# Performance work log

Hardware: AMD Instinct MI355X
Metric: run time of the kernel (lower is better)

The kernel has to match this reference:

```python
import jax, jax.numpy as jnp
import numpy as np

EPS = 1e-5  # BatchNorm eps


def _bn(x, g, b, axes):
    # training-mode batch norm over `axes`, channel dim broadcast via g/b shape
    m = jnp.mean(x, axis=axes, keepdims=True)
    v = jnp.var(x, axis=axes, keepdims=True)
    shape = [1] * x.ndim
    ch_axis = [a for a in range(x.ndim) if a not in axes][0]
    shape[ch_axis] = g.shape[0]
    return g.reshape(shape) * (x - m) * jax.lax.rsqrt(v + EPS) + b.reshape(shape)


def setup_inputs() -> dict:
    key = jax.random.key(0)
    ks = jax.random.split(key, 8)
    B, C, N = 16, 3, 2048

    def w(k_, fan_in, fan_out):
        return jax.random.normal(k_, (fan_in, fan_out), jnp.float32) * (1.0 / np.sqrt(fan_in))

    return {
        "pc": jax.random.normal(ks[0], (B, C, N), jnp.float32),
        "W1": w(ks[1], 6, 64), "g1": jnp.ones(64), "b1": jnp.zeros(64),
        "W2": w(ks[2], 64, 128), "g2": jnp.ones(128), "b2": jnp.zeros(128),
        "W3": w(ks[3], 128, 1024), "g3": jnp.ones(1024), "b3": jnp.zeros(1024),
        "Wf1": w(ks[4], 1024, 512), "gf1": jnp.ones(512), "bf1": jnp.zeros(512),
        "Wf2": w(ks[5], 512, 256), "gf2": jnp.ones(256), "bf2": jnp.zeros(256),
        "Wf3": jnp.zeros((256, 9), jnp.float32),           # zero-initialized per source
        "bf3": jnp.eye(3, dtype=jnp.float32).reshape(-1),  # identity bias per source
        "k": 20,
    }


def reference(pc, W1, g1, b1, W2, g2, b2, W3, g3, b3,
              Wf1, gf1, bf1, Wf2, gf2, bf2, Wf3, bf3, k):
    B, C, N = pc.shape
    # ---- KNN graph on coordinates (B x C x N) ----
    sq = jnp.sum(pc * pc, axis=1)                      # B,N
    inner = jnp.einsum('bcn,bcm->bnm', pc, pc)         # B,N,N
    negdist = 2.0 * inner - sq[:, :, None] - sq[:, None, :]
    _, idx = jax.lax.top_k(negdist, k)                 # B,N,k (includes self)
    # gather neighbor features: f (C,N), i (N,k) -> (C,N,k)
    topk = jax.vmap(lambda f, i: f[:, i])(pc, idx)     # B,C,N,k
    center = pc[:, :, :, None]
    edge = jnp.concatenate(
        [jnp.broadcast_to(center, topk.shape), topk - center], axis=1)  # B,2C,N,k

    # ---- edge conv (1x1 conv + BN + ReLU), pool=False ----
    h = jnp.einsum('bcnk,co->bonk', edge, W1)
    h = jax.nn.relu(_bn(h, g1, b1, (0, 2, 3)))         # B,64,N,k
    # ---- conv2 then max over k ----
    h = jnp.einsum('bcnk,co->bonk', h, W2)
    h = jax.nn.relu(_bn(h, g2, b2, (0, 2, 3)))         # B,128,N,k
    h = jnp.max(h, axis=-1)                            # B,128,N
    # ---- conv3 then max over N ----
    h = jnp.einsum('bcn,co->bon', h, W3)
    h = jax.nn.relu(_bn(h, g3, b3, (0, 2)))            # B,1024,N
    h = jnp.max(h, axis=-1)                            # B,1024
    # ---- FC stack ----
    h = jax.nn.relu(_bn(h @ Wf1, gf1, bf1, (0,)))      # B,512
    h = jax.nn.relu(_bn(h @ Wf2, gf2, bf2, (0,)))      # B,256
    h = h @ Wf3 + bf3                                  # B,9
    return h.reshape(B, 3, 3)
```

## Files before the change

kernel.cpp:

```cpp
#include <hip/hip_runtime.h>
#include <math.h>

#define Nn 2048

#define OFF_IDX    ((size_t)0)
#define OFF_P2MAX  (((size_t)4)  << 20)
#define OFF_P2MIN  (((size_t)13) << 20)
#define OFF_PS2    (((size_t)22) << 20)
#define OFF_PQ2    (((size_t)23) << 20)
#define OFF_STATS  (((size_t)24) << 20)
#define OFF_MOM    (OFF_STATS + 0)
#define OFF_A1C1   (OFF_STATS + 4096)
#define OFF_A2C2   (OFF_STATS + 8192)
#define OFF_S3SUM  (OFF_STATS + 12288)
#define OFF_S3SQ   (OFF_STATS + 20480)
#define OFF_P3MAX  (OFF_STATS + 28672)
#define OFF_P3MIN  (OFF_STATS + 94208)
#define OFF_R3     (OFF_STATS + 159744)
#define OFF_R4     (OFF_STATS + 225280)
#define OFF_R5     (OFF_STATS + 258048)
#define OFF_DOTS1  (OFF_STATS + 274432)
#define OFF_DOTS2  (OFF_STATS + 307200)
#define OFF_W2BF   (OFF_STATS + 323584)
#define OFF_W3BF   (OFF_STATS + 339968)
#define WS_NEEDED  (OFF_STATS + 602112)

typedef __attribute__((ext_vector_type(8))) short bf16x8;
typedef __attribute__((ext_vector_type(4))) float f32x4;

__device__ __forceinline__ unsigned fkey(float f){
  unsigned u = __float_as_uint(f);
  return (u & 0x80000000u) ? ~u : (u | 0x80000000u);
}
__device__ __forceinline__ float fdec(unsigned k){
  unsigned u = (k & 0x80000000u) ? (k & 0x7FFFFFFFu) : ~k;
  return __uint_as_float(u);
}
__device__ __forceinline__ short f2bf(float x){
  unsigned u = __float_as_uint(x);
  u += 0x7fffu + ((u >> 16) & 1u);
  return (short)(u >> 16);
}
__device__ __forceinline__ float bf2f(short v){
  return __uint_as_float(((unsigned)(unsigned short)v) << 16);
}
__device__ __forceinline__ float med3(float a, float b, float c){
  float d;
  asm("v_med3_f32 %0, %1, %2, %3" : "=v"(d) : "v"(a), "v"(b), "v"(c));
  return d;
}
__device__ __forceinline__ float ndist(float tQx, float tQy, float tQz, float Qw, float4 P){
  return fmaf(tQx, P.x, fmaf(tQy, P.y, fmaf(tQz, P.z, -Qw - P.w)));
}
__device__ __forceinline__ void insert20(float (&m)[20], float x){
  #pragma unroll
  for (int t = 0; t < 19; t++) m[t] = med3(m[t], m[t+1], x);
  m[19] = fmaxf(m[19], x);
}

__global__ __launch_bounds__(256) void k_init(char* __restrict__ ws){
  int i = blockIdx.x*256 + threadIdx.x;
  if (i < 7168) ((unsigned*)(ws + OFF_MOM))[i] = 0u;
  if (i < 16384){
    ((unsigned*)(ws + OFF_P3MAX))[i] = 0u;
    ((unsigned*)(ws + OFF_P3MIN))[i] = 0xFFFFFFFFu;
  }
  if (i < 12288) ((float*)(ws + OFF_DOTS1))[i] = 0.f;
}

__global__ __launch_bounds__(256) void k_castw(const float* __restrict__ W2,
      const float* __restrict__ W3, short* __restrict__ W2BF,
      short* __restrict__ W3BF){
  int id = blockIdx.x*256 + threadIdx.x;
  if (id < 16384){
    int q = id >> 4, k0 = (id & 15)*8;
    bf16x8 vv;
    #pragma unroll
    for (int j = 0; j < 8; j++) vv[j] = f2bf(W3[(size_t)(k0+j)*1024 + q]);
    *(bf16x8*)&W3BF[q*128 + k0] = vv;
  } else if (id < 17408){
    int id2 = id - 16384;
    int q = id2 >> 3, k0 = (id2 & 7)*8;
    bf16x8 vv;
    #pragma unroll
    for (int j = 0; j < 8; j++) vv[j] = f2bf(W2[(k0+j)*128 + q]);
    *(bf16x8*)&W2BF[q*64 + k0] = vv;
  }
}

__global__ __launch_bounds__(512) void k_knn(const float* __restrict__ pc,
                                             int* __restrict__ idxg,
                                             double* __restrict__ MOM){
  __shared__ float4 pts[Nn];
  __shared__ unsigned cnt[64];
  __shared__ float momS[27];
  const int tid = threadIdx.x;
  const int b = blockIdx.y;
  const int n0 = blockIdx.x*64;
  const float* pcb = pc + b*3*Nn;
  for (int i = tid; i < Nn; i += 512){
    float x = pcb[i], y = pcb[Nn+i], z = pcb[2*Nn+i];
    pts[i] = make_float4(x, y, z, x*x + y*y + z*z);
  }
  if (tid < 64) cnt[tid] = 0u;
  if (tid < 27) momS[tid] = 0.f;
  __syncthreads();

  const int ql = tid >> 3, c = tid & 7;
  const int n = n0 + ql;
  const float4 Q = pts[n];
  const float tQx = 2.f*Q.x, tQy = 2.f*Q.y, tQz = 2.f*Q.z;

  float v[20];
  #pragma unroll
  for (int t = 0; t < 20; t++) v[t] = -3.4e38f;
  #pragma unroll 1
  for (int i = 0; i < 256; i += 4){
    float4 P0 = pts[(i+0)*8 + c];
    float4 P1 = pts[(i+1)*8 + c];
    float4 P2 = pts[(i+2)*8 + c];
    float4 P3 = pts[(i+3)*8 + c];
    insert20(v, ndist(tQx, tQy, tQz, Q.w, P0));
    insert20(v, ndist(tQx, tQy, tQz, Q.w, P1));
    insert20(v, ndist(tQx, tQy, tQz, Q.w, P2));
    insert20(v, ndist(tQx, tQy, tQz, Q.w, P3));
  }

  #pragma unroll
  for (int stage = 4; stage >= 1; stage >>= 1){
    float w[20];
    #pragma unroll
    for (int t = 0; t < 20; t++) w[t] = __shfl_xor(v[t], stage);
    #pragma unroll
    for (int t = 0; t < 20; t++) insert20(v, w[t]);
  }
  const float th = v[0];

  int* myidx = &idxg[((size_t)((b<<11) + n))*20];
  #pragma unroll 1
  for (int i = 0; i < 256; i += 4){
    float4 P0 = pts[(i+0)*8 + c];
    float4 P1 = pts[(i+1)*8 + c];
    float4 P2 = pts[(i+2)*8 + c];
    float4 P3 = pts[(i+3)*8 + c];
    float nd0 = ndist(tQx, tQy, tQz, Q.w, P0);
    float nd1 = ndist(tQx, tQy, tQz, Q.w, P1);
    float nd2 = ndist(tQx, tQy, tQz, Q.w, P2);
    float nd3 = ndist(tQx, tQy, tQz, Q.w, P3);
    if (nd0 >= th){ unsigned p = atomicAdd(&cnt[ql], 1u); if (p < 20u) myidx[p] = (i+0)*8 + c; }
    if (nd1 >= th){ unsigned p = atomicAdd(&cnt[ql], 1u); if (p < 20u) myidx[p] = (i+1)*8 + c; }
    if (nd2 >= th){ unsigned p = atomicAdd(&cnt[ql], 1u); if (p < 20u) myidx[p] = (i+2)*8 + c; }
    if (nd3 >= th){ unsigned p = atomicAdd(&cnt[ql], 1u); if (p < 20u) myidx[p] = (i+3)*8 + c; }
  }
  __threadfence_block();
  __syncthreads();

  if (c == 0){
    unsigned have = cnt[ql]; if (have > 20u) have = 20u;
    for (unsigned p = have; p < 20u; ++p) myidx[p] = n;
  }
  __threadfence_block();
  __syncthreads();

  float s1[6] = {0,0,0,0,0,0};
  float s2[21] = {0,0,0,0,0,0,0,0,0,0,0,0,0,0,0,0,0,0,0,0,0};
  #pragma unroll 1
  for (int j = tid; j < 1280; j += 512){
    int q = j/20, t = j - q*20;
    int m = idxg[((size_t)((b<<11) + n0 + q))*20 + t] & 2047;
    float4 P = pts[m];
    float4 Qq = pts[n0 + q];
    float e[6] = {Qq.x, Qq.y, Qq.z, P.x - Qq.x, P.y - Qq.y, P.z - Qq.z};
    int u = 0;
    #pragma unroll
    for (int a = 0; a < 6; a++){
      s1[a] += e[a];
      #pragma unroll
      for (int bq = a; bq < 6; bq++){ s2[u] += e[a]*e[bq]; u++; }
    }
  }
  #pragma unroll
  for (int a = 0; a < 6; a++)
    for (int off = 32; off > 0; off >>= 1) s1[a] += __shfl_xor(s1[a], off);
  #pragma unroll
  for (int u = 0; u < 21; u++)
    for (int off = 32; off > 0; off >>= 1) s2[u] += __shfl_xor(s2[u], off);
  if ((tid & 63) == 0){
    #pragma unroll
    for (int a = 0; a < 6; a++) atomicAdd(&momS[a], s1[a]);
    #pragma unroll
    for (int u = 0; u < 21; u++) atomicAdd(&momS[6+u], s2[u]);
  }
  __syncthreads();
  if (tid < 27) atomicAdd(&MOM[tid], (double)momS[tid]);
}

__global__ __launch_bounds__(64) void k_coef1(const double* __restrict__ MOM,
        const float* __restrict__ W1, const float* __restrict__ g1,
        const float* __restrict__ b1, float* __restrict__ A1C1){
  const int o = threadIdx.x;
  const double inv = 1.0/655360.0;
  double w[6]; double m = 0.0;
  #pragma unroll
  for (int c = 0; c < 6; c++){ w[c] = (double)W1[c*64+o]; m += w[c]*MOM[c]*inv; }
  double e2 = 0.0; int u = 0;
  #pragma unroll
  for (int c = 0; c < 6; c++){
    #pragma unroll
    for (int cp = c; cp < 6; cp++){
      double mm = MOM[6+u]*inv; u++;
      e2 += (c == cp) ? w[c]*w[c]*mm : 2.0*w[c]*w[cp]*mm;
    }
  }
  double var = e2 - m*m;
  double a = (double)g1[o] / sqrt(var + 1e-5);
  #pragma unroll
  for (int c = 0; c < 6; c++) A1C1[c*64+o] = (float)(a*w[c]);
  A1C1[384+o] = (float)((double)b1[o] - a*m);
}

__global__ __launch_bounds__(256) void k_conv12(const float* __restrict__ pc,
      const int* __restrict__ idxg, const float* __restrict__ A1C1,
      const short* __restrict__ W2BF,
      float* __restrict__ PS2, float* __restrict__ PQ2,
      short* __restrict__ P2MAX, short* __restrict__ P2MIN){
  __shared__ float es[6][512];
  __shared__ short h1s[512*64];
  __shared__ float w1s[448];
  __shared__ float ssum[128], ssq[128];
  const int tid = threadIdx.x;
  const int b = blockIdx.y;
  const int n0 = blockIdx.x*16;
  const float* pcb = pc + b*3*Nn;

  for (int i = tid; i < 448; i += 256) w1s[i] = A1C1[i];

  for (int s = tid; s < 512; s += 256){
    int nl = s >> 5, kk = s & 31;
    int n = n0 + nl;
    int kke = (kk < 20) ? kk : 0;
    int m = idxg[((size_t)((b<<11)+n))*20 + kke] & 2047;
    float cx = pcb[n],  cy = pcb[Nn+n],  cz = pcb[2*Nn+n];
    float px = pcb[m],  py = pcb[Nn+m],  pz = pcb[2*Nn+m];
    es[0][s] = cx;    es[1][s] = cy;    es[2][s] = cz;
    es[3][s] = px-cx; es[4][s] = py-cy; es[5][s] = pz-cz;
  }
  __syncthreads();

  for (int i = tid; i < 4096; i += 256){
    int s = i >> 3, oc = i & 7;
    bf16x8 hv;
    #pragma unroll
    for (int j = 0; j < 8; j++){
      int o = oc*8 + j;
      float acc = w1s[384 + o];
      #pragma unroll
      for (int c = 0; c < 6; c++) acc = fmaf(w1s[c*64 + o], es[c][s], acc);
      hv[j] = f2bf(fmaxf(acc, 0.f));
    }
    *(bf16x8*)&h1s[s*64 + ((oc ^ (s & 7)) << 3)] = hv;
  }
  __syncthreads();

  const int l = tid & 63, wv = tid >> 6;
  const int col = l & 15, kc = l >> 4;

  bf16x8 Bf[2][2];
  #pragma unroll
  for (int qt = 0; qt < 2; qt++){
    int q = wv*32 + qt*16 + col;
    #pragma unroll
    for (int ks = 0; ks < 2; ks++)
      Bf[qt][ks] = *(const bf16x8*)&W2BF[q*64 + ks*32 + kc*8];
  }

  float smacc[2] = {0.f, 0.f}, sqacc[2] = {0.f, 0.f};
  const bool t1real = (kc == 0);

  #pragma unroll 1
  for (int g = 0; g < 16; g++){
    bf16x8 Af[2][2];
    #pragma unroll
    for (int t = 0; t < 2; t++){
      int row = g*32 + t*16 + col;
      #pragma unroll
      for (int ks = 0; ks < 2; ks++){
        int chunk = (ks*4 + kc) ^ (row & 7);
        Af[t][ks] = *(const bf16x8*)&h1s[row*64 + chunk*8];
      }
    }
    #pragma unroll
    for (int qt = 0; qt < 2; qt++){
      f32x4 a0 = {0.f,0.f,0.f,0.f}, a1 = {0.f,0.f,0.f,0.f};
      a0 = __builtin_amdgcn_mfma_f32_16x16x32_bf16(Af[0][0], Bf[qt][0], a0, 0,0,0);
      a0 = __builtin_amdgcn_mfma_f32_16x16x32_bf16(Af[0][1], Bf[qt][1], a0, 0,0,0);
      a1 = __builtin_amdgcn_mfma_f32_16x16x32_bf16(Af[1][0], Bf[qt][0], a1, 0,0,0);
      a1 = __builtin_amdgcn_mfma_f32_16x16x32_bf16(Af[1][1], Bf[qt][1], a1, 0,0,0);
      float mx = a0[0], mn = a0[0], sm = 0.f, sq = 0.f;
      #pragma unroll
      for (int r = 0; r < 4; r++){
        float v0 = a0[r], v1 = a1[r];
        mx = fmaxf(mx, fmaxf(v0, v1));
        mn = fminf(mn, fminf(v0, v1));
        sm += v0; sq += v0*v0;
      }
      if (t1real){
        #pragma unroll
        for (int r = 0; r < 4; r++){ float v1 = a1[r]; sm += v1; sq += v1*v1; }
      }
      smacc[qt] += sm; sqacc[qt] += sq;
      mx = fmaxf(mx, __shfl_xor(mx, 16)); mx = fmaxf(mx, __shfl_xor(mx, 32));
      mn = fminf(mn, __shfl_xor(mn, 16)); mn = fminf(mn, __shfl_xor(mn, 32));
      if (kc == 0){
        size_t base = ((size_t)(b*Nn + n0 + g))*128 + (size_t)(wv*32 + qt*16 + col);
        P2MAX[base] = f2bf(mx);
        P2MIN[base] = f2bf(mn);
      }
    }
  }
  #pragma unroll
  for (int qt = 0; qt < 2; qt++){
    smacc[qt] += __shfl_xor(smacc[qt], 16); smacc[qt] += __shfl_xor(smacc[qt], 32);
    sqacc[qt] += __shfl_xor(sqacc[qt], 16); sqacc[qt] += __shfl_xor(sqacc[qt], 32);
    if (kc == 0){
      ssum[wv*32 + qt*16 + col] = smacc[qt];
      ssq [wv*32 + qt*16 + col] = sqacc[qt];
    }
  }
  __syncthreads();
  if (tid < 128){
    int bid = b*128 + blockIdx.x;
    PS2[tid*2048 + bid] = ssum[tid];
    PQ2[tid*2048 + bid] = ssq[tid];
  }
}

__global__ __launch_bounds__(256) void k_coef2(const float* __restrict__ PS2,
        const float* __restrict__ PQ2, const float* __restrict__ g2,
        const float* __restrict__ b2, float* __restrict__ A2C2){
  __shared__ float sred[4], qred[4];
  const int p = blockIdx.x;
  const int tid = threadIdx.x;
  float s = 0.f, q = 0.f;
  for (int i = tid; i < 2048; i += 256){ s += PS2[p*2048 + i]; q += PQ2[p*2048 + i]; }
  #pragma unroll
  for (int off = 32; off > 0; off >>= 1){ s += __shfl_xor(s, off); q += __shfl_xor(q, off); }
  if ((tid & 63) == 0){ sred[tid >> 6] = s; qred[tid >> 6] = q; }
  __syncthreads();
  if (tid == 0){
    double sum = (double)sred[0] + sred[1] + sred[2] + sred[3];
    double sq  = (double)qred[0] + qred[1] + qred[2] + qred[3];
    double mean = sum * (1.0/655360.0);
    double var  = sq  * (1.0/655360.0) - mean*mean;
    double a = (double)g2[p] / sqrt(var + 1e-5);
    A2C2[p]     = (float)a;
    A2C2[128+p] = (float)((double)b2[p] - a*mean);
  }
}

__global__ __launch_bounds__(256) void k_conv3(const short* __restrict__ P2MAX,
      const short* __restrict__ P2MIN, const float* __restrict__ A2C2,
      const short* __restrict__ W3BF, double* __restrict__ S3SUM,
      double* __restrict__ S3SQ, unsigned* __restrict__ P3MAX,
      unsigned* __restrict__ P3MIN){
  __shared__ short As[128*128];
  __shared__ float a2[128], c2[128];
  const int tid = threadIdx.x;
  const int b = blockIdx.y;
  const int n0 = blockIdx.x*128;
  const int qh = blockIdx.z;
  if (tid < 128){ a2[tid] = A2C2[tid]; c2[tid] = A2C2[128+tid]; }
  __syncthreads();

  for (int idx = tid; idx < 2048; idx += 256){
    int s = idx >> 4, oc = idx & 15;
    size_t base = ((size_t)(b*Nn + n0 + s))*128 + (size_t)(oc*8);
    bf16x8 vmx = *(const bf16x8*)&P2MAX[base];
    bf16x8 vmn = *(const bf16x8*)&P2MIN[base];
    bf16x8 vv;
    #pragma unroll
    for (int j = 0; j < 8; j++){
      int o = oc*8 + j;
      float aa = a2[o];
      float vsel = bf2f((aa >= 0.f) ? vmx[j] : vmn[j]);
      vv[j] = f2bf(fmaxf(aa*vsel + c2[o], 0.f));
    }
    int chunk = oc ^ (s & 7);
    *(bf16x8*)&As[s*128 + chunk*8] = vv;
  }
  __syncthreads();

  const int l = tid & 63, wv = tid >> 6;
  const int col = l & 15, kc = l >> 4;

  #pragma unroll 1
  for (int pass = 0; pass < 2; ++pass){
    bf16x8 Bf[4][4];
    #pragma unroll
    for (int qt = 0; qt < 4; qt++){
      int q = qh*512 + wv*128 + pass*64 + qt*16 + col;
      #pragma unroll
      for (int ks = 0; ks < 4; ks++)
        Bf[qt][ks] = *(const bf16x8*)&W3BF[q*128 + ks*32 + kc*8];
    }
    float smx[4], smn[4], ssm[4], ssqv[4];
    #pragma unroll
    for (int qt = 0; qt < 4; qt++){ smx[qt] = -3.4e38f; smn[qt] = 3.4e38f; ssm[qt] = 0.f; ssqv[qt] = 0.f; }

    #pragma unroll 1
    for (int st = 0; st < 8; ++st){
      bf16x8 Af[4];
      int row = st*16 + col;
      #pragma unroll
      for (int ks = 0; ks < 4; ks++){
        int chunk = (ks*4 + kc) ^ (row & 7);
        Af[ks] = *(const bf16x8*)&As[row*128 + chunk*8];
      }
      #pragma unroll
      for (int qt = 0; qt < 4; qt++){
        f32x4 acc = {0.f, 0.f, 0.f, 0.f};
        #pragma unroll
        for (int ks = 0; ks < 4; ks++)
          acc = __builtin_amdgcn_mfma_f32_16x16x32_bf16(Af[ks], Bf[qt][ks], acc, 0, 0, 0);
        #pragma unroll
        for (int r = 0; r < 4; r++){
          float vv = acc[r];
          smx[qt] = fmaxf(smx[qt], vv); smn[qt] = fminf(smn[qt], vv);
          ssm[qt] += vv; ssqv[qt] += vv*vv;
        }
      }
    }
    #pragma unroll
    for (int qt = 0; qt < 4; qt++){
      #pragma unroll
      for (int off = 16; off <= 32; off <<= 1){
        smx[qt] = fmaxf(smx[qt], __shfl_xor(smx[qt], off));
        smn[qt] = fminf(smn[qt], __shfl_xor(smn[qt], off));
        ssm[qt] += __shfl_xor(ssm[qt], off);
        ssqv[qt] += __shfl_xor(ssqv[qt], off);
      }
    }
    if (kc == 0){
      #pragma unroll
      for (int qt = 0; qt < 4; qt++){
        int q = qh*512 + wv*128 + pass*64 + qt*16 + col;
        atomicMax(&P3MAX[b*1024 + q], fkey(smx[qt]));
        atomicMin(&P3MIN[b*1024 + q], fkey(smn[qt]));
        atomicAdd(&S3SUM[q], (double)ssm[qt]);
        atomicAdd(&S3SQ[q],  (double)ssqv[qt]);
      }
    }
  }
}

__global__ __launch_bounds__(256) void k_bn3relu(const double* __restrict__ S3SUM,
      const double* __restrict__ S3SQ, const unsigned* __restrict__ P3MAX,
      const unsigned* __restrict__ P3MIN, const float* __restrict__ g3,
      const float* __restrict__ b3, float* __restrict__ R3){
  int id = blockIdx.x*256 + threadIdx.x;
  int q = id & 1023;
  double mean = S3SUM[q] * (1.0/32768.0);
  double var  = S3SQ[q] * (1.0/32768.0) - mean*mean;
  double a = (double)g3[q] / sqrt(var + 1e-5);
  double c = (double)b3[q] - a*mean;
  float v = fdec((a >= 0.0) ? P3MAX[id] : P3MIN[id]);
  R3[id] = fmaxf((float)(a*(double)v + c), 0.f);
}

template<int IN, int OUT>
__global__ __launch_bounds__(256) void k_fcdot(const float* __restrict__ X,
      const float* __restrict__ W, float* __restrict__ dots){
  constexpr int L = IN/16;
  __shared__ float Xs[16*L];
  const int tid = threadIdx.x;
  const int o = blockIdx.x*64 + (tid & 63);
  const int wv = tid >> 6;
  const int c0 = blockIdx.y*L;
  for (int i = tid; i < 16*L; i += 256){
    int bb = i / L, cc = i - bb*L;
    Xs[i] = X[bb*IN + c0 + cc];
  }
  __syncthreads();
  constexpr int CPW = L/4;
  float acc[16];
  #pragma unroll
  for (int bb = 0; bb < 16; bb++) acc[bb] = 0.f;
  for (int cc = wv*CPW; cc < (wv+1)*CPW; ++cc){
    float w = W[(size_t)(c0+cc)*OUT + o];
    #pragma unroll
    for (int bb = 0; bb < 16; bb++) acc[bb] += Xs[bb*L + cc]*w;
  }
  #pragma unroll
  for (int bb = 0; bb < 16; bb++) atomicAdd(&dots[bb*OUT + o], acc[bb]);
}

template<int OUT>
__global__ __launch_bounds__(64) void k_fcbn(const float* __restrict__ dots,
      const float* __restrict__ g, const float* __restrict__ bet,
      float* __restrict__ Y){
  const int o = blockIdx.x*64 + threadIdx.x;
  float d[16]; float m = 0.f;
  #pragma unroll
  for (int bb = 0; bb < 16; bb++){ d[bb] = dots[bb*OUT + o]; m += d[bb]; }
  m *= (1.f/16.f);
  float v = 0.f;
  #pragma unroll
  for (int bb = 0; bb < 16; bb++){ float x = d[bb]-m; v += x*x; }
  v *= (1.f/16.f);
  float a = g[o] * rsqrtf(v + 1e-5f);
  #pragma unroll
  for (int bb = 0; bb < 16; bb++) Y[bb*OUT + o] = fmaxf(a*(d[bb]-m) + bet[o], 0.f);
}

__global__ __launch_bounds__(192) void k_head(const float* __restrict__ R5,
      const float* __restrict__ Wf3, const float* __restrict__ bf3,
      float* __restrict__ out){
  int t = threadIdx.x;
  if (t >= 144) return;
  int b = t/9, j = t - b*9;
  float acc = bf3[j];
  for (int c = 0; c < 256; c++) acc += R5[b*256 + c]*Wf3[c*9 + j];
  out[t] = acc;
}

extern "C" void kernel_launch(void* const* d_in, const int* in_sizes, int n_in,
                              void* d_out, int out_size, void* d_ws, size_t ws_size,
                              hipStream_t stream) {
  if (ws_size < WS_NEEDED) return;
  const float* pc  = (const float*)d_in[0];
  const float* W1  = (const float*)d_in[1];
  const float* g1  = (const float*)d_in[2];
  const float* b1  = (const float*)d_in[3];
  const float* W2  = (const float*)d_in[4];
  const float* g2  = (const float*)d_in[5];
  const float* b2  = (const float*)d_in[6];
  const float* W3  = (const float*)d_in[7];
  const float* g3  = (const float*)d_in[8];
  const float* b3  = (const float*)d_in[9];
  const float* Wf1 = (const float*)d_in[10];
  const float* gf1 = (const float*)d_in[11];
  const float* bf1 = (const float*)d_in[12];
  const float* Wf2 = (const float*)d_in[13];
  const float* gf2 = (const float*)d_in[14];
  const float* bf2 = (const float*)d_in[15];
  const float* Wf3 = (const float*)d_in[16];
  const float* bf3 = (const float*)d_in[17];

  char* ws = (char*)d_ws;
  int*      IDX   = (int*)     (ws + OFF_IDX);
  short*    P2MAXp= (short*)   (ws + OFF_P2MAX);
  short*    P2MINp= (short*)   (ws + OFF_P2MIN);
  float*    PS2p  = (float*)   (ws + OFF_PS2);
  float*    PQ2p  = (float*)   (ws + OFF_PQ2);
  double*   MOMp  = (double*)  (ws + OFF_MOM);
  float*    A1C1p = (float*)   (ws + OFF_A1C1);
  float*    A2C2p = (float*)   (ws + OFF_A2C2);
  double*   S3SUMp= (double*)  (ws + OFF_S3SUM);
  double*   S3SQp = (double*)  (ws + OFF_S3SQ);
  unsigned* P3MAXp= (unsigned*)(ws + OFF_P3MAX);
  unsigned* P3MINp= (unsigned*)(ws + OFF_P3MIN);
  float*    R3p   = (float*)   (ws + OFF_R3);
  float*    R4p   = (float*)   (ws + OFF_R4);
  float*    R5p   = (float*)   (ws + OFF_R5);
  float*    DOTS1p= (float*)   (ws + OFF_DOTS1);
  float*    DOTS2p= (float*)   (ws + OFF_DOTS2);
  short*    W2BFp = (short*)   (ws + OFF_W2BF);
  short*    W3BFp = (short*)   (ws + OFF_W3BF);

  k_init          <<<dim3(64),       256, 0, stream>>>(ws);
  k_castw         <<<dim3(68),       256, 0, stream>>>(W2, W3, W2BFp, W3BFp);
  k_knn           <<<dim3(32,16),    512, 0, stream>>>(pc, IDX, MOMp);
  k_coef1         <<<dim3(1),         64, 0, stream>>>(MOMp, W1, g1, b1, A1C1p);
  k_conv12        <<<dim3(128,16),   256, 0, stream>>>(pc, IDX, A1C1p, W2BFp, PS2p, PQ2p, P2MAXp, P2MINp);
  k_coef2         <<<dim3(128),      256, 0, stream>>>(PS2p, PQ2p, g2, b2, A2C2p);
  k_conv3         <<<dim3(16,16,2),  256, 0, stream>>>(P2MAXp, P2MINp, A2C2p, W3BFp, S3SUMp, S3SQp, P3MAXp, P3MINp);
  k_bn3relu       <<<dim3(64),       256, 0, stream>>>(S3SUMp, S3SQp, P3MAXp, P3MINp, g3, b3, R3p);
  k_fcdot<1024,512><<<dim3(8,16),    256, 0, stream>>>(R3p, Wf1, DOTS1p);
  k_fcbn<512>     <<<dim3(8),         64, 0, stream>>>(DOTS1p, gf1, bf1, R4p);
  k_fcdot<512,256><<<dim3(4,16),     256, 0, stream>>>(R4p, Wf2, DOTS2p);
  k_fcbn<256>     <<<dim3(4),         64, 0, stream>>>(DOTS2p, gf2, bf2, R5p);
  k_head          <<<dim3(1),        192, 0, stream>>>(R5p, Wf3, bf3, (float*)d_out);
}
```

Baseline: 238.0 us.

## Fuse small kernels and halve conv12 shared-memory footprint via chunked h1

```diff
diff --git a/kernel.cpp b/kernel.cpp
--- a/kernel.cpp
+++ b/kernel.cpp
@@ -10,15 +10,11 @@
 #define OFF_PQ2    (((size_t)23) << 20)
 #define OFF_STATS  (((size_t)24) << 20)
 #define OFF_MOM    (OFF_STATS + 0)
-#define OFF_A1C1   (OFF_STATS + 4096)
 #define OFF_A2C2   (OFF_STATS + 8192)
 #define OFF_S3SUM  (OFF_STATS + 12288)
 #define OFF_S3SQ   (OFF_STATS + 20480)
 #define OFF_P3MAX  (OFF_STATS + 28672)
 #define OFF_P3MIN  (OFF_STATS + 94208)
-#define OFF_R3     (OFF_STATS + 159744)
-#define OFF_R4     (OFF_STATS + 225280)
-#define OFF_R5     (OFF_STATS + 258048)
 #define OFF_DOTS1  (OFF_STATS + 274432)
 #define OFF_DOTS2  (OFF_STATS + 307200)
 #define OFF_W2BF   (OFF_STATS + 323584)
@@ -58,7 +54,9 @@
   m[19] = fmaxf(m[19], x);
 }
 
-__global__ __launch_bounds__(256) void k_init(char* __restrict__ ws){
+__global__ __launch_bounds__(256) void k_setup(char* __restrict__ ws,
+      const float* __restrict__ W2, const float* __restrict__ W3,
+      short* __restrict__ W2BF, short* __restrict__ W3BF){
   int i = blockIdx.x*256 + threadIdx.x;
   if (i < 7168) ((unsigned*)(ws + OFF_MOM))[i] = 0u;
   if (i < 16384){
@@ -66,20 +64,14 @@
     ((unsigned*)(ws + OFF_P3MIN))[i] = 0xFFFFFFFFu;
   }
   if (i < 12288) ((float*)(ws + OFF_DOTS1))[i] = 0.f;
-}
-
-__global__ __launch_bounds__(256) void k_castw(const float* __restrict__ W2,
-      const float* __restrict__ W3, short* __restrict__ W2BF,
-      short* __restrict__ W3BF){
-  int id = blockIdx.x*256 + threadIdx.x;
-  if (id < 16384){
-    int q = id >> 4, k0 = (id & 15)*8;
+  if (i < 16384){
+    int q = i >> 4, k0 = (i & 15)*8;
     bf16x8 vv;
     #pragma unroll
     for (int j = 0; j < 8; j++) vv[j] = f2bf(W3[(size_t)(k0+j)*1024 + q]);
     *(bf16x8*)&W3BF[q*128 + k0] = vv;
-  } else if (id < 17408){
-    int id2 = id - 16384;
+  } else if (i < 17408){
+    int id2 = i - 16384;
     int q = id2 >> 3, k0 = (id2 & 7)*8;
     bf16x8 vv;
     #pragma unroll
@@ -195,37 +187,14 @@
   if (tid < 27) atomicAdd(&MOM[tid], (double)momS[tid]);
 }
 
-__global__ __launch_bounds__(64) void k_coef1(const double* __restrict__ MOM,
-        const float* __restrict__ W1, const float* __restrict__ g1,
-        const float* __restrict__ b1, float* __restrict__ A1C1){
-  const int o = threadIdx.x;
-  const double inv = 1.0/655360.0;
-  double w[6]; double m = 0.0;
-  #pragma unroll
-  for (int c = 0; c < 6; c++){ w[c] = (double)W1[c*64+o]; m += w[c]*MOM[c]*inv; }
-  double e2 = 0.0; int u = 0;
-  #pragma unroll
-  for (int c = 0; c < 6; c++){
-    #pragma unroll
-    for (int cp = c; cp < 6; cp++){
-      double mm = MOM[6+u]*inv; u++;
-      e2 += (c == cp) ? w[c]*w[c]*mm : 2.0*w[c]*w[cp]*mm;
-    }
-  }
-  double var = e2 - m*m;
-  double a = (double)g1[o] / sqrt(var + 1e-5);
-  #pragma unroll
-  for (int c = 0; c < 6; c++) A1C1[c*64+o] = (float)(a*w[c]);
-  A1C1[384+o] = (float)((double)b1[o] - a*m);
-}
-
 __global__ __launch_bounds__(256) void k_conv12(const float* __restrict__ pc,
-      const int* __restrict__ idxg, const float* __restrict__ A1C1,
-      const short* __restrict__ W2BF,
+      const int* __restrict__ idxg, const double* __restrict__ MOM,
+      const float* __restrict__ W1, const float* __restrict__ g1,
+      const float* __restrict__ b1, const short* __restrict__ W2BF,
       float* __restrict__ PS2, float* __restrict__ PQ2,
       short* __restrict__ P2MAX, short* __restrict__ P2MIN){
   __shared__ float es[6][512];
-  __shared__ short h1s[512*64];
+  __shared__ short h1s[256*64];
   __shared__ float w1s[448];
   __shared__ float ssum[128], ssq[128];
   const int tid = threadIdx.x;
@@ -233,7 +202,27 @@
   const int n0 = blockIdx.x*16;
   const float* pcb = pc + b*3*Nn;
 
-  for (int i = tid; i < 448; i += 256) w1s[i] = A1C1[i];
+  if (tid < 64){
+    const int o = tid;
+    const double inv = 1.0/655360.0;
+    double w[6]; double m = 0.0;
+    #pragma unroll
+    for (int cc = 0; cc < 6; cc++){ w[cc] = (double)W1[cc*64+o]; m += w[cc]*MOM[cc]*inv; }
+    double e2 = 0.0; int u = 0;
+    #pragma unroll
+    for (int cc = 0; cc < 6; cc++){
+      #pragma unroll
+      for (int cp = cc; cp < 6; cp++){
+        double mm = MOM[6+u]*inv; u++;
+        e2 += (cc == cp) ? w[cc]*w[cc]*mm : 2.0*w[cc]*w[cp]*mm;
+      }
+    }
+    double var = e2 - m*m;
+    double a = (double)g1[o] / sqrt(var + 1e-5);
+    #pragma unroll
+    for (int cc = 0; cc < 6; cc++) w1s[cc*64+o] = (float)(a*w[cc]);
+    w1s[384+o] = (float)((double)b1[o] - a*m);
+  }
 
   for (int s = tid; s < 512; s += 256){
     int nl = s >> 5, kk = s & 31;
@@ -247,21 +236,6 @@
   }
   __syncthreads();
 
-  for (int i = tid; i < 4096; i += 256){
-    int s = i >> 3, oc = i & 7;
-    bf16x8 hv;
-    #pragma unroll
-    for (int j = 0; j < 8; j++){
-      int o = oc*8 + j;
-      float acc = w1s[384 + o];
-      #pragma unroll
-      for (int c = 0; c < 6; c++) acc = fmaf(w1s[c*64 + o], es[c][s], acc);
-      hv[j] = f2bf(fmaxf(acc, 0.f));
-    }
-    *(bf16x8*)&h1s[s*64 + ((oc ^ (s & 7)) << 3)] = hv;
-  }
-  __syncthreads();
-
   const int l = tid & 63, wv = tid >> 6;
   const int col = l & 15, kc = l >> 4;
 
@@ -278,46 +252,68 @@
   const bool t1real = (kc == 0);
 
   #pragma unroll 1
-  for (int g = 0; g < 16; g++){
-    bf16x8 Af[2][2];
-    #pragma unroll
-    for (int t = 0; t < 2; t++){
-      int row = g*32 + t*16 + col;
-      #pragma unroll
-      for (int ks = 0; ks < 2; ks++){
-        int chunk = (ks*4 + kc) ^ (row & 7);
-        Af[t][ks] = *(const bf16x8*)&h1s[row*64 + chunk*8];
-      }
-    }
-    #pragma unroll
-    for (int qt = 0; qt < 2; qt++){
-      f32x4 a0 = {0.f,0.f,0.f,0.f}, a1 = {0.f,0.f,0.f,0.f};
-      a0 = __builtin_amdgcn_mfma_f32_16x16x32_bf16(Af[0][0], Bf[qt][0], a0, 0,0,0);
-      a0 = __builtin_amdgcn_mfma_f32_16x16x32_bf16(Af[0][1], Bf[qt][1], a0, 0,0,0);
-      a1 = __builtin_amdgcn_mfma_f32_16x16x32_bf16(Af[1][0], Bf[qt][0], a1, 0,0,0);
-      a1 = __builtin_amdgcn_mfma_f32_16x16x32_bf16(Af[1][1], Bf[qt][1], a1, 0,0,0);
-      float mx = a0[0], mn = a0[0], sm = 0.f, sq = 0.f;
-      #pragma unroll
-      for (int r = 0; r < 4; r++){
-        float v0 = a0[r], v1 = a1[r];
-        mx = fmaxf(mx, fmaxf(v0, v1));
-        mn = fminf(mn, fminf(v0, v1));
-        sm += v0; sq += v0*v0;
-      }
-      if (t1real){
+  for (int ch = 0; ch < 2; ch++){
+    for (int i = tid; i < 2048; i += 256){
+      int sl = i >> 3, oc = i & 7;
+      int s = (ch << 8) + sl;
+      bf16x8 hv;
+      #pragma unroll
+      for (int j = 0; j < 8; j++){
+        int o = oc*8 + j;
+        float acc = w1s[384 + o];
         #pragma unroll
-        for (int r = 0; r < 4; r++){ float v1 = a1[r]; sm += v1; sq += v1*v1; }
-      }
-      smacc[qt] += sm; sqacc[qt] += sq;
-      mx = fmaxf(mx, __shfl_xor(mx, 16)); mx = fmaxf(mx, __shfl_xor(mx, 32));
-      mn = fminf(mn, __shfl_xor(mn, 16)); mn = fminf(mn, __shfl_xor(mn, 32));
-      if (kc == 0){
-        size_t base = ((size_t)(b*Nn + n0 + g))*128 + (size_t)(wv*32 + qt*16 + col);
-        P2MAX[base] = f2bf(mx);
-        P2MIN[base] = f2bf(mn);
-      }
-    }
-  }
+        for (int cc = 0; cc < 6; cc++) acc = fmaf(w1s[cc*64 + o], es[cc][s], acc);
+        hv[j] = f2bf(fmaxf(acc, 0.f));
+      }
+      *(bf16x8*)&h1s[sl*64 + ((oc ^ (sl & 7)) << 3)] = hv;
+    }
+    __syncthreads();
+
+    #pragma unroll 1
+    for (int g2 = 0; g2 < 8; g2++){
+      const int g = ch*8 + g2;
+      bf16x8 Af[2][2];
+      #pragma unroll
+      for (int t = 0; t < 2; t++){
+        int rl = g2*32 + t*16 + col;
+        #pragma unroll
+        for (int ks = 0; ks < 2; ks++){
+          int chunk = (ks*4 + kc) ^ (rl & 7);
+          Af[t][ks] = *(const bf16x8*)&h1s[rl*64 + chunk*8];
+        }
+      }
+      #pragma unroll
+      for (int qt = 0; qt < 2; qt++){
+        f32x4 a0 = {0.f,0.f,0.f,0.f}, a1 = {0.f,0.f,0.f,0.f};
+        a0 = __builtin_amdgcn_mfma_f32_16x16x32_bf16(Af[0][0], Bf[qt][0], a0, 0,0,0);
+        a0 = __builtin_amdgcn_mfma_f32_16x16x32_bf16(Af[0][1], Bf[qt][1], a0, 0,0,0);
+        a1 = __builtin_amdgcn_mfma_f32_16x16x32_bf16(Af[1][0], Bf[qt][0], a1, 0,0,0);
+        a1 = __builtin_amdgcn_mfma_f32_16x16x32_bf16(Af[1][1], Bf[qt][1], a1, 0,0,0);
+        float mx = a0[0], mn = a0[0], sm = 0.f, sq = 0.f;
+        #pragma unroll
+        for (int r = 0; r < 4; r++){
+          float v0 = a0[r], v1 = a1[r];
+          mx = fmaxf(mx, fmaxf(v0, v1));
+          mn = fminf(mn, fminf(v0, v1));
+          sm += v0; sq += v0*v0;
+        }
+        if (t1real){
+          #pragma unroll
+          for (int r = 0; r < 4; r++){ float v1 = a1[r]; sm += v1; sq += v1*v1; }
+        }
+        smacc[qt] += sm; sqacc[qt] += sq;
+        mx = fmaxf(mx, __shfl_xor(mx, 16)); mx = fmaxf(mx, __shfl_xor(mx, 32));
+        mn = fminf(mn, __shfl_xor(mn, 16)); mn = fminf(mn, __shfl_xor(mn, 32));
+        if (kc == 0){
+          size_t base = ((size_t)(b*Nn + n0 + g))*128 + (size_t)(wv*32 + qt*16 + col);
+          P2MAX[base] = f2bf(mx);
+          P2MIN[base] = f2bf(mn);
+        }
+      }
+    }
+    __syncthreads();
+  }
+
   #pragma unroll
   for (int qt = 0; qt < 2; qt++){
     smacc[qt] += __shfl_xor(smacc[qt], 16); smacc[qt] += __shfl_xor(smacc[qt], 32);
@@ -453,74 +449,104 @@
   }
 }
 
-__global__ __launch_bounds__(256) void k_bn3relu(const double* __restrict__ S3SUM,
+__global__ __launch_bounds__(256) void k_fc1(const double* __restrict__ S3SUM,
       const double* __restrict__ S3SQ, const unsigned* __restrict__ P3MAX,
       const unsigned* __restrict__ P3MIN, const float* __restrict__ g3,
-      const float* __restrict__ b3, float* __restrict__ R3){
-  int id = blockIdx.x*256 + threadIdx.x;
-  int q = id & 1023;
-  double mean = S3SUM[q] * (1.0/32768.0);
-  double var  = S3SQ[q] * (1.0/32768.0) - mean*mean;
-  double a = (double)g3[q] / sqrt(var + 1e-5);
-  double c = (double)b3[q] - a*mean;
-  float v = fdec((a >= 0.0) ? P3MAX[id] : P3MIN[id]);
-  R3[id] = fmaxf((float)(a*(double)v + c), 0.f);
-}
-
-template<int IN, int OUT>
-__global__ __launch_bounds__(256) void k_fcdot(const float* __restrict__ X,
-      const float* __restrict__ W, float* __restrict__ dots){
-  constexpr int L = IN/16;
-  __shared__ float Xs[16*L];
+      const float* __restrict__ b3, const float* __restrict__ Wf1,
+      float* __restrict__ dots){
+  __shared__ float Xs[16*64];
   const int tid = threadIdx.x;
   const int o = blockIdx.x*64 + (tid & 63);
-  const int wv = tid >> 6;
-  const int c0 = blockIdx.y*L;
-  for (int i = tid; i < 16*L; i += 256){
-    int bb = i / L, cc = i - bb*L;
-    Xs[i] = X[bb*IN + c0 + cc];
-  }
-  __syncthreads();
-  constexpr int CPW = L/4;
+  const int wvv = tid >> 6;
+  const int c0 = blockIdx.y*64;
+  for (int i = tid; i < 1024; i += 256){
+    int bb = i >> 6, cc = i & 63;
+    int q = c0 + cc;
+    int id = bb*1024 + q;
+    double mean = S3SUM[q] * (1.0/32768.0);
+    double var  = S3SQ[q] * (1.0/32768.0) - mean*mean;
+    double a = (double)g3[q] / sqrt(var + 1e-5);
+    double cbn = (double)b3[q] - a*mean;
+    float v = fdec((a >= 0.0) ? P3MAX[id] : P3MIN[id]);
+    Xs[bb*64 + cc] = fmaxf((float)(a*(double)v + cbn), 0.f);
+  }
+  __syncthreads();
   float acc[16];
   #pragma unroll
   for (int bb = 0; bb < 16; bb++) acc[bb] = 0.f;
-  for (int cc = wv*CPW; cc < (wv+1)*CPW; ++cc){
-    float w = W[(size_t)(c0+cc)*OUT + o];
-    #pragma unroll
-    for (int bb = 0; bb < 16; bb++) acc[bb] += Xs[bb*L + cc]*w;
-  }
-  #pragma unroll
-  for (int bb = 0; bb < 16; bb++) atomicAdd(&dots[bb*OUT + o], acc[bb]);
-}
-
-template<int OUT>
-__global__ __launch_bounds__(64) void k_fcbn(const float* __restrict__ dots,
-      const float* __restrict__ g, const float* __restrict__ bet,
-      float* __restrict__ Y){
-  const int o = blockIdx.x*64 + threadIdx.x;
-  float d[16]; float m = 0.f;
-  #pragma unroll
-  for (int bb = 0; bb < 16; bb++){ d[bb] = dots[bb*OUT + o]; m += d[bb]; }
-  m *= (1.f/16.f);
-  float v = 0.f;
-  #pragma unroll
-  for (int bb = 0; bb < 16; bb++){ float x = d[bb]-m; v += x*x; }
-  v *= (1.f/16.f);
-  float a = g[o] * rsqrtf(v + 1e-5f);
-  #pragma unroll
-  for (int bb = 0; bb < 16; bb++) Y[bb*OUT + o] = fmaxf(a*(d[bb]-m) + bet[o], 0.f);
-}
-
-__global__ __launch_bounds__(192) void k_head(const float* __restrict__ R5,
+  for (int cc = wvv*16; cc < wvv*16 + 16; ++cc){
+    float w = Wf1[(size_t)(c0+cc)*512 + o];
+    #pragma unroll
+    for (int bb = 0; bb < 16; bb++) acc[bb] += Xs[bb*64 + cc]*w;
+  }
+  #pragma unroll
+  for (int bb = 0; bb < 16; bb++) atomicAdd(&dots[bb*512 + o], acc[bb]);
+}
+
+__global__ __launch_bounds__(256) void k_fc2(const float* __restrict__ DOTS1,
+      const float* __restrict__ gf1, const float* __restrict__ bf1,
+      const float* __restrict__ Wf2, float* __restrict__ dots){
+  __shared__ float Xs[16*32];
+  const int tid = threadIdx.x;
+  const int o = blockIdx.x*64 + (tid & 63);
+  const int wvv = tid >> 6;
+  const int c0 = blockIdx.y*32;
+  if (tid < 32){
+    int o1 = c0 + tid;
+    float d[16]; float m = 0.f;
+    #pragma unroll
+    for (int bb = 0; bb < 16; bb++){ d[bb] = DOTS1[bb*512 + o1]; m += d[bb]; }
+    m *= (1.f/16.f);
+    float vv = 0.f;
+    #pragma unroll
+    for (int bb = 0; bb < 16; bb++){ float x = d[bb]-m; vv += x*x; }
+    vv *= (1.f/16.f);
+    float a = gf1[o1] * rsqrtf(vv + 1e-5f);
+    #pragma unroll
+    for (int bb = 0; bb < 16; bb++)
+      Xs[bb*32 + tid] = fmaxf(a*(d[bb]-m) + bf1[o1], 0.f);
+  }
+  __syncthreads();
+  float acc[16];
+  #pragma unroll
+  for (int bb = 0; bb < 16; bb++) acc[bb] = 0.f;
+  for (int cc = wvv*8; cc < wvv*8 + 8; ++cc){
+    float w = Wf2[(size_t)(c0+cc)*256 + o];
+    #pragma unroll
+    for (int bb = 0; bb < 16; bb++) acc[bb] += Xs[bb*32 + cc]*w;
+  }
+  #pragma unroll
+  for (int bb = 0; bb < 16; bb++) atomicAdd(&dots[bb*256 + o], acc[bb]);
+}
+
+__global__ __launch_bounds__(256) void k_head(const float* __restrict__ DOTS2,
+      const float* __restrict__ gf2, const float* __restrict__ bf2,
       const float* __restrict__ Wf3, const float* __restrict__ bf3,
       float* __restrict__ out){
-  int t = threadIdx.x;
-  if (t >= 144) return;
-  int b = t/9, j = t - b*9;
-  float acc = bf3[j];
-  for (int c = 0; c < 256; c++) acc += R5[b*256 + c]*Wf3[c*9 + j];
-  out[t] = acc;
+  __shared__ float R5s[16*256];
+  const int tid = threadIdx.x;
+  {
+    int o = tid;
+    float d[16]; float m = 0.f;
+    #pragma unroll
+    for (int bb = 0; bb < 16; bb++){ d[bb] = DOTS2[bb*256 + o]; m += d[bb]; }
+    m *= (1.f/16.f);
+    float vv = 0.f;
+    #pragma unroll
+    for (int bb = 0; bb < 16; bb++){ float x = d[bb]-m; vv += x*x; }
+    vv *= (1.f/16.f);
+    float a = gf2[o] * rsqrtf(vv + 1e-5f);
+    #pragma unroll
+    for (int bb = 0; bb < 16; bb++)
+      R5s[bb*256 + o] = fmaxf(a*(d[bb]-m) + bf2[o], 0.f);
+  }
+  __syncthreads();
+  if (tid < 144){
+    int b = tid/9, j = tid - b*9;
+    float acc = bf3[j];
+    for (int cq = 0; cq < 256; cq++) acc += R5s[b*256 + cq]*Wf3[cq*9 + j];
+    out[tid] = acc;
+  }
 }
 
 extern "C" void kernel_launch(void* const* d_in, const int* in_sizes, int n_in,
@@ -553,31 +579,22 @@
   float*    PS2p  = (float*)   (ws + OFF_PS2);
   float*    PQ2p  = (float*)   (ws + OFF_PQ2);
   double*   MOMp  = (double*)  (ws + OFF_MOM);
-  float*    A1C1p = (float*)   (ws + OFF_A1C1);
   float*    A2C2p = (float*)   (ws + OFF_A2C2);
   double*   S3SUMp= (double*)  (ws + OFF_S3SUM);
   double*   S3SQp = (double*)  (ws + OFF_S3SQ);
   unsigned* P3MAXp= (unsigned*)(ws + OFF_P3MAX);
   unsigned* P3MINp= (unsigned*)(ws + OFF_P3MIN);
-  float*    R3p   = (float*)   (ws + OFF_R3);
-  float*    R4p   = (float*)   (ws + OFF_R4);
-  float*    R5p   = (float*)   (ws + OFF_R5);
   float*    DOTS1p= (float*)   (ws + OFF_DOTS1);
   float*    DOTS2p= (float*)   (ws + OFF_DOTS2);
   short*    W2BFp = (short*)   (ws + OFF_W2BF);
   short*    W3BFp = (short*)   (ws + OFF_W3BF);
 
-  k_init          <<<dim3(64),       256, 0, stream>>>(ws);
-  k_castw         <<<dim3(68),       256, 0, stream>>>(W2, W3, W2BFp, W3BFp);
-  k_knn           <<<dim3(32,16),    512, 0, stream>>>(pc, IDX, MOMp);
-  k_coef1         <<<dim3(1),         64, 0, stream>>>(MOMp, W1, g1, b1, A1C1p);
-  k_conv12        <<<dim3(128,16),   256, 0, stream>>>(pc, IDX, A1C1p, W2BFp, PS2p, PQ2p, P2MAXp, P2MINp);
-  k_coef2         <<<dim3(128),      256, 0, stream>>>(PS2p, PQ2p, g2, b2, A2C2p);
-  k_conv3         <<<dim3(16,16,2),  256, 0, stream>>>(P2MAXp, P2MINp, A2C2p, W3BFp, S3SUMp, S3SQp, P3MAXp, P3MINp);
-  k_bn3relu       <<<dim3(64),       256, 0, stream>>>(S3SUMp, S3SQp, P3MAXp, P3MINp, g3, b3, R3p);
-  k_fcdot<1024,512><<<dim3(8,16),    256, 0, stream>>>(R3p, Wf1, DOTS1p);
-  k_fcbn<512>     <<<dim3(8),         64, 0, stream>>>(DOTS1p, gf1, bf1, R4p);
-  k_fcdot<512,256><<<dim3(4,16),     256, 0, stream>>>(R4p, Wf2, DOTS2p);
-  k_fcbn<256>     <<<dim3(4),         64, 0, stream>>>(DOTS2p, gf2, bf2, R5p);
-  k_head          <<<dim3(1),        192, 0, stream>>>(R5p, Wf3, bf3, (float*)d_out);
-}
+  k_setup <<<dim3(68),      256, 0, stream>>>(ws, W2, W3, W2BFp, W3BFp);
+  k_knn   <<<dim3(32,16),   512, 0, stream>>>(pc, IDX, MOMp);
+  k_conv12<<<dim3(128,16),  256, 0, stream>>>(pc, IDX, MOMp, W1, g1, b1, W2BFp, PS2p, PQ2p, P2MAXp, P2MINp);
+  k_coef2 <<<dim3(128),     256, 0, stream>>>(PS2p, PQ2p, g2, b2, A2C2p);
+  k_conv3 <<<dim3(16,16,2), 256, 0, stream>>>(P2MAXp, P2MINp, A2C2p, W3BFp, S3SUMp, S3SQp, P3MAXp, P3MINp);
+  k_fc1   <<<dim3(8,16),    256, 0, stream>>>(S3SUMp, S3SQp, P3MAXp, P3MINp, g3, b3, Wf1, DOTS1p);
+  k_fc2   <<<dim3(4,16),    256, 0, stream>>>(DOTS1p, gf1, bf1, Wf2, DOTS2p);
+  k_head  <<<dim3(1),       256, 0, stream>>>(DOTS2p, gf2, bf2, Wf3, bf3, (float*)d_out);
+}
```

Result: faster. 214.6 us (-9.8%).
